# Kernel tuning notes

Hardware: AMD Instinct MI355X
Metric: run time of the kernel (lower is better)

## Reference

```python
import jax, jax.numpy as jnp
import numpy as np

BN_EPS = 1e-5


def _interpolate(xyz1, xyz2, points2):
    # squared pairwise distances [B, N, S]
    d = (jnp.sum(xyz1 ** 2, -1)[:, :, None]
         + jnp.sum(xyz2 ** 2, -1)[:, None, :]
         - 2.0 * jnp.einsum('bnc,bsc->bns', xyz1, xyz2))
    # 3 smallest distances (torch does a full sort; top-3 is the same math)
    neg_d, idx = jax.lax.top_k(-d, 3)          # [B, N, 3]
    dists = -neg_d
    w = 1.0 / (dists + 1e-8)
    w = w / jnp.sum(w, -1, keepdims=True)
    # gather points2 features at idx: [B, N, 3, D]
    gathered = jnp.take_along_axis(points2[:, None, :, :],
                                   idx[:, :, :, None], axis=2)
    return jnp.sum(gathered * w[:, :, :, None], axis=2)  # [B, N, D]


def _conv_bn_relu(x, w, b, gamma, beta):
    # x: [B, N, Cin]; 1x1 Conv1d == per-point dense layer
    y = jnp.einsum('bnc,oc->bno', x, w) + b
    mean = jnp.mean(y, axis=(0, 1))
    var = jnp.mean((y - mean) ** 2, axis=(0, 1))  # biased var (torch BN training)
    y = (y - mean) * jax.lax.rsqrt(var + BN_EPS) * gamma + beta
    return jax.nn.relu(y)


def setup_inputs() -> dict:
    key = jax.random.key(0)
    ks = jax.random.split(key, 8)
    B, N, S, D1, D2 = 8, 8192, 2048, 128, 256
    in_ch, mlp = D1 + D2, [256, 128]
    inp = {
        'xyz1': jax.random.normal(ks[0], (B, N, 3), jnp.float32),
        'xyz2': jax.random.normal(ks[1], (B, S, 3), jnp.float32),
        'points1': jax.random.normal(ks[2], (B, N, D1), jnp.float32),
        'points2': jax.random.normal(ks[3], (B, S, D2), jnp.float32),
    }
    c = in_ch
    for i, o in enumerate(mlp):
        kw = jax.random.fold_in(ks[4], i)
        inp[f'w{i}'] = jax.random.normal(kw, (o, c), jnp.float32) * (1.0 / np.sqrt(c))
        inp[f'b{i}'] = jnp.zeros((o,), jnp.float32)
        inp[f'g{i}'] = jnp.ones((o,), jnp.float32)
        inp[f'beta{i}'] = jnp.zeros((o,), jnp.float32)
        c = o
    return inp


def reference(xyz1, xyz2, points1, points2,
              w0, b0, g0, beta0, w1, b1, g1, beta1):
    interp = _interpolate(xyz1, xyz2, points2)          # [B, N, D2]
    x = jnp.concatenate([points1, interp], axis=-1)     # [B, N, D1+D2]
    x = _conv_bn_relu(x, w0, b0, g0, beta0)
    x = _conv_bn_relu(x, w1, b1, g1, beta1)
    return x                                            # [B, N, mlp[-1]]
```

## Files before the change

kernel.cpp:

```cpp
#include <hip/hip_runtime.h>
#include <hip/hip_bf16.h>

#define BATCH 8
#define NPTS  8192
#define SPTS  2048
#define D1C   128
#define D2C   256
#define C_IN  384
#define O0    256
#define O1    128
#define MROWS (BATCH * NPTS)
#define NCHUNK 8
#define CHSZ   256

typedef __attribute__((ext_vector_type(8))) short short8v;
typedef __attribute__((ext_vector_type(4))) float f32x4;

__device__ __forceinline__ unsigned short f2bf(float f) {
    union { float f; unsigned u; } v; v.f = f;
    unsigned u = v.u;
    return (unsigned short)((u + 0x7fffu + ((u >> 16) & 1u)) >> 16);
}
__device__ __forceinline__ float bf2f(unsigned short h) {
    union { unsigned u; float f; } v; v.u = ((unsigned)h) << 16;
    return v.f;
}
__device__ __forceinline__ void gload_lds16(const void* g, void* l) {
    __builtin_amdgcn_global_load_lds(
        (const __attribute__((address_space(1))) void*)g,
        (__attribute__((address_space(3))) void*)l, 16, 0, 0);
}

__global__ __launch_bounds__(256, 8) void nn3_scan(
    const float* __restrict__ xyz1, const float* __restrict__ xyz2,
    float* __restrict__ candD, int* __restrict__ candI)
{
    __shared__ float4 P[CHSZ];
    const int t  = threadIdx.x;
    const int qb = blockIdx.x;
    const int c  = blockIdx.y;
    const int b  = qb >> 5;

    {
        const float* src = xyz2 + ((size_t)b * SPTS + c * CHSZ) * 3;
        float px = src[t * 3 + 0];
        float py = src[t * 3 + 1];
        float pz = src[t * 3 + 2];
        P[t] = make_float4(px, py, pz, px * px + py * py + pz * pz);
    }
    __syncthreads();

    const int q = qb * 256 + t;
    const float* qp = xyz1 + (size_t)q * 3;
    const float qx = qp[0], qy = qp[1], qz = qp[2];
    const float qn = qx * qx + qy * qy + qz * qz;

    float d0 = 1e30f, d1 = 1e30f, d2 = 1e30f;
    int   i0 = 0,     i1 = 0,     i2 = 0;
    const int gbase = c * CHSZ;

    #pragma unroll 4
    for (int s = 0; s < CHSZ; ++s) {
        float4 p = P[s];
        float dot = qx * p.x + qy * p.y + qz * p.z;
        float d = (qn + p.w) - 2.0f * dot;
        bool c0 = d < d0, c1 = d < d1, c2 = d < d2;
        int gi = gbase + s;
        float t2 = __builtin_amdgcn_fmed3f(d, d1, d2);
        float t1 = __builtin_amdgcn_fmed3f(d, d0, d1);
        i2 = c1 ? i1 : (c2 ? gi : i2);
        i1 = c0 ? i0 : (c1 ? gi : i1);
        i0 = c0 ? gi : i0;
        d2 = t2; d1 = t1; d0 = fminf(d, d0);
    }

    const size_t base = (size_t)c * (MROWS * 3) + (size_t)q * 3;
    candD[base + 0] = d0; candD[base + 1] = d1; candD[base + 2] = d2;
    candI[base + 0] = i0; candI[base + 1] = i1; candI[base + 2] = i2;
}

__global__ __launch_bounds__(256) void nn3_merge(
    const float* __restrict__ candD, const int* __restrict__ candI,
    int* __restrict__ idx3, float* __restrict__ wgt3)
{
    const int q = blockIdx.x * 256 + threadIdx.x;

    float d0 = 1e30f, d1 = 1e30f, d2 = 1e30f;
    int   i0 = 0,     i1 = 0,     i2 = 0;

    #pragma unroll
    for (int c = 0; c < NCHUNK; ++c) {
        const size_t base = (size_t)c * (MROWS * 3) + (size_t)q * 3;
        #pragma unroll
        for (int j = 0; j < 3; ++j) {
            float d = candD[base + j];
            int  gi = candI[base + j];
            bool c0 = d < d0, c1 = d < d1, c2 = d < d2;
            float t2 = __builtin_amdgcn_fmed3f(d, d1, d2);
            float t1 = __builtin_amdgcn_fmed3f(d, d0, d1);
            i2 = c1 ? i1 : (c2 ? gi : i2);
            i1 = c0 ? i0 : (c1 ? gi : i1);
            i0 = c0 ? gi : i0;
            d2 = t2; d1 = t1; d0 = fminf(d, d0);
        }
    }

    float wa = 1.0f / (d0 + 1e-8f);
    float wb = 1.0f / (d1 + 1e-8f);
    float wc = 1.0f / (d2 + 1e-8f);
    float inv = 1.0f / (wa + wb + wc);
    wa *= inv; wb *= inv; wc *= inv;

    idx3[q * 3 + 0] = i0;
    idx3[q * 3 + 1] = i1;
    idx3[q * 3 + 2] = i2;
    wgt3[q * 3 + 0] = wa;
    wgt3[q * 3 + 1] = wb;
    wgt3[q * 3 + 2] = wc;
}

__global__ __launch_bounds__(256) void cvt_f32_bf16(
    const float* __restrict__ src, unsigned short* __restrict__ dst)
{
    int i = blockIdx.x * 256 + threadIdx.x;
    float4 v = ((const float4*)src)[i];
    ushort4 o;
    o.x = f2bf(v.x); o.y = f2bf(v.y); o.z = f2bf(v.z); o.w = f2bf(v.w);
    ((ushort4*)dst)[i] = o;
}

__global__ __launch_bounds__(256) void interp_kernel(
    const float* __restrict__ points2,
    const int* __restrict__ idx3, const float* __restrict__ wgt3,
    unsigned short* __restrict__ xI)
{
    const int w    = threadIdx.x >> 6;
    const int lane = threadIdx.x & 63;
    const int blk   = blockIdx.x;
    const int xcd   = blk & 7;
    const int local = blk >> 3;
    const int m     = (xcd * 2048 + local) * 4 + w;
    const int b     = xcd;

    const float* p2b = points2 + (size_t)b * SPTS * D2C;
    const int  gi0 = idx3[m * 3 + 0];
    const int  gi1 = idx3[m * 3 + 1];
    const int  gi2 = idx3[m * 3 + 2];
    const float w0 = wgt3[m * 3 + 0];
    const float w1 = wgt3[m * 3 + 1];
    const float w2 = wgt3[m * 3 + 2];

    float4 a  = *(const float4*)(p2b + (size_t)gi0 * D2C + lane * 4);
    float4 bb = *(const float4*)(p2b + (size_t)gi1 * D2C + lane * 4);
    float4 c  = *(const float4*)(p2b + (size_t)gi2 * D2C + lane * 4);

    ushort4 o;
    o.x = f2bf(w0 * a.x + w1 * bb.x + w2 * c.x);
    o.y = f2bf(w0 * a.y + w1 * bb.y + w2 * c.y);
    o.z = f2bf(w0 * a.z + w1 * bb.z + w2 * c.z);
    o.w = f2bf(w0 * a.w + w1 * bb.w + w2 * c.w);
    *(ushort4*)(xI + (size_t)m * D2C + lane * 4) = o;
}

__global__ __launch_bounds__(512) void gemm0_mfma(
    const float* __restrict__ points1, const unsigned short* __restrict__ xI,
    const unsigned short* __restrict__ w0bf, const float* __restrict__ b0,
    unsigned short* __restrict__ y0bf,
    float* __restrict__ sum0, float* __restrict__ sq0)
{
    __shared__ __align__(16) unsigned short As[128 * 32];
    __shared__ __align__(16) unsigned short Bs[256 * 32];

    const int t    = threadIdx.x;
    const int lane = t & 63;
    const int w    = t >> 6;
    const int wm   = w >> 2;
    const int wn   = w & 3;
    const int rowBase = blockIdx.x * 128;

    const int r      = t >> 2;
    const int ks_log = (t & 3) ^ ((t >> 3) & 3);

    const float* p1row = points1 + (size_t)(rowBase + r) * D1C;
    const unsigned short* xrow = xI + (size_t)(rowBase + r) * D2C + ks_log * 8;
    unsigned short* asw = As + t * 8;
    char* ldsA = (char*)As + w * 1024;

    const unsigned short* gB0 = w0bf + (size_t)r * C_IN + ks_log * 8;
    const unsigned short* gB1 = w0bf + (size_t)(128 + r) * C_IN + ks_log * 8;
    char* ldsB0 = (char*)Bs + w * 1024;
    char* ldsB1 = (char*)Bs + 8192 + w * 1024;

    const int rp = (lane & 15) * 64 + (((lane >> 4) ^ ((lane >> 1) & 3)) * 16);
    const char* aBase = (const char*)As + (wm * 64) * 64 + rp;
    const char* bBase = (const char*)Bs + (wn * 64) * 64 + rp;

    f32x4 acc[4][4] = {};

    for (int kt = 0; kt < C_IN / 32; ++kt) {
        gload_lds16(gB0 + kt * 32, ldsB0);
        gload_lds16(gB1 + kt * 32, ldsB1);

        if (kt < 4) {
            const int k = kt * 32 + ks_log * 8;
            float4 f0 = *(const float4*)(p1row + k);
            float4 f1 = *(const float4*)(p1row + k + 4);
            short8v av;
            av[0] = (short)f2bf(f0.x); av[1] = (short)f2bf(f0.y);
            av[2] = (short)f2bf(f0.z); av[3] = (short)f2bf(f0.w);
            av[4] = (short)f2bf(f1.x); av[5] = (short)f2bf(f1.y);
            av[6] = (short)f2bf(f1.z); av[7] = (short)f2bf(f1.w);
            *(short8v*)asw = av;
        } else {
            gload_lds16(xrow + (kt - 4) * 32, ldsA);
        }

        __syncthreads();

        short8v a[4], bf[4];
        #pragma unroll
        for (int m = 0; m < 4; ++m) a[m]  = *(const short8v*)(aBase + m * 1024);
        #pragma unroll
        for (int n = 0; n < 4; ++n) bf[n] = *(const short8v*)(bBase + n * 1024);
        #pragma unroll
        for (int m = 0; m < 4; ++m)
            #pragma unroll
            for (int n = 0; n < 4; ++n)
                acc[m][n] = __builtin_amdgcn_mfma_f32_16x16x32_bf16(
                    a[m], bf[n], acc[m][n], 0, 0, 0);

        __syncthreads();
    }

    const int colw = wn * 64 + (lane & 15);
    const int rowE = rowBase + wm * 64 + ((lane >> 4) * 4);
    float bias[4];
    #pragma unroll
    for (int n = 0; n < 4; ++n) bias[n] = b0[colw + n * 16];

    float cs[4] = {0.f, 0.f, 0.f, 0.f}, cq[4] = {0.f, 0.f, 0.f, 0.f};
    #pragma unroll
    for (int m = 0; m < 4; ++m)
        #pragma unroll
        for (int n = 0; n < 4; ++n)
            #pragma unroll
            for (int j = 0; j < 4; ++j) {
                float v = acc[m][n][j] + bias[n];
                y0bf[(size_t)(rowE + m * 16 + j) * O0 + colw + n * 16] = f2bf(v);
                cs[n] += v; cq[n] += v * v;
            }

    #pragma unroll
    for (int n = 0; n < 4; ++n) {
        float s = cs[n], qv = cq[n];
        s  += __shfl_xor(s, 16);  s  += __shfl_xor(s, 32);
        qv += __shfl_xor(qv, 16); qv += __shfl_xor(qv, 32);
        if (lane < 16) {
            atomicAdd(&sum0[colw + n * 16], s);
            atomicAdd(&sq0[colw + n * 16], qv);
        }
    }
}

__global__ void stats_kernel(const float* __restrict__ sum, const float* __restrict__ sq,
                             const float* __restrict__ g, const float* __restrict__ beta,
                             float* __restrict__ scale, float* __restrict__ shift,
                             int C, float invM)
{
    int c = blockIdx.x * blockDim.x + threadIdx.x;
    if (c < C) {
        float mean = sum[c] * invM;
        float var  = sq[c] * invM - mean * mean;
        float s = g[c] * rsqrtf(var + 1e-5f);
        scale[c] = s;
        shift[c] = beta[c] - mean * s;
    }
}

__global__ __launch_bounds__(256) void gemm1_mfma(
    const unsigned short* __restrict__ x1, const unsigned short* __restrict__ w1bf,
    const float* __restrict__ scale0, const float* __restrict__ shift0,
    const float* __restrict__ b1, unsigned short* __restrict__ y1bf,
    float* __restrict__ sum1, float* __restrict__ sq1)
{
    __shared__ __align__(16) unsigned short As[128 * 32];
    __shared__ __align__(16) unsigned short Bs[128 * 32];
    __shared__ float sc[O0], sh[O0];

    const int t    = threadIdx.x;
    const int lane = t & 63;
    const int w    = t >> 6;
    const int wm   = w >> 1, wn = w & 1;
    const int rowBase = blockIdx.x * 128;

    sc[t] = scale0[t];
    sh[t] = shift0[t];
    __syncthreads();

    const int r      = t >> 2;
    const int kl     = t & 3;
    const int kp     = kl ^ ((r >> 1) & 3);
    const int ks_log = kl ^ ((r >> 1) & 3);

    const unsigned short* gA0 = x1 + (size_t)(rowBase + r) * O0 + kl * 8;
    const unsigned short* gA1 = x1 + (size_t)(rowBase + 64 + r) * O0 + kl * 8;
    unsigned short* dA0 = As + r * 32 + kp * 8;
    unsigned short* dA1 = As + (64 + r) * 32 + kp * 8;

    const unsigned short* gB0 = w1bf + (size_t)r * O0 + ks_log * 8;
    const unsigned short* gB1 = w1bf + (size_t)(64 + r) * O0 + ks_log * 8;
    char* ldsB0 = (char*)Bs + w * 1024;
    char* ldsB1 = (char*)Bs + 4096 + w * 1024;

    const int rp = (lane & 15) * 64 + (((lane >> 4) ^ ((lane >> 1) & 3)) * 16);
    const char* aBase = (const char*)As + (wm * 64) * 64 + rp;
    const char* bBase = (const char*)Bs + (wn * 64) * 64 + rp;

    f32x4 acc[4][4] = {};

    for (int kt = 0; kt < O0 / 32; ++kt) {
        gload_lds16(gB0 + kt * 32, ldsB0);
        gload_lds16(gB1 + kt * 32, ldsB1);

        const int ch = kt * 32 + kl * 8;
        float4 s0v = *(const float4*)(sc + ch);
        float4 s1v = *(const float4*)(sc + ch + 4);
        float4 h0v = *(const float4*)(sh + ch);
        float4 h1v = *(const float4*)(sh + ch + 4);
        short8v v0 = *(const short8v*)(gA0 + kt * 32);
        short8v v1 = *(const short8v*)(gA1 + kt * 32);
        short8v o0, o1;
        o0[0] = (short)f2bf(fmaxf(0.f, bf2f((unsigned short)v0[0]) * s0v.x + h0v.x));
        o0[1] = (short)f2bf(fmaxf(0.f, bf2f((unsigned short)v0[1]) * s0v.y + h0v.y));
        o0[2] = (short)f2bf(fmaxf(0.f, bf2f((unsigned short)v0[2]) * s0v.z + h0v.z));
        o0[3] = (short)f2bf(fmaxf(0.f, bf2f((unsigned short)v0[3]) * s0v.w + h0v.w));
        o0[4] = (short)f2bf(fmaxf(0.f, bf2f((unsigned short)v0[4]) * s1v.x + h1v.x));
        o0[5] = (short)f2bf(fmaxf(0.f, bf2f((unsigned short)v0[5]) * s1v.y + h1v.y));
        o0[6] = (short)f2bf(fmaxf(0.f, bf2f((unsigned short)v0[6]) * s1v.z + h1v.z));
        o0[7] = (short)f2bf(fmaxf(0.f, bf2f((unsigned short)v0[7]) * s1v.w + h1v.w));
        o1[0] = (short)f2bf(fmaxf(0.f, bf2f((unsigned short)v1[0]) * s0v.x + h0v.x));
        o1[1] = (short)f2bf(fmaxf(0.f, bf2f((unsigned short)v1[1]) * s0v.y + h0v.y));
        o1[2] = (short)f2bf(fmaxf(0.f, bf2f((unsigned short)v1[2]) * s0v.z + h0v.z));
        o1[3] = (short)f2bf(fmaxf(0.f, bf2f((unsigned short)v1[3]) * s0v.w + h0v.w));
        o1[4] = (short)f2bf(fmaxf(0.f, bf2f((unsigned short)v1[4]) * s1v.x + h1v.x));
        o1[5] = (short)f2bf(fmaxf(0.f, bf2f((unsigned short)v1[5]) * s1v.y + h1v.y));
        o1[6] = (short)f2bf(fmaxf(0.f, bf2f((unsigned short)v1[6]) * s1v.z + h1v.z));
        o1[7] = (short)f2bf(fmaxf(0.f, bf2f((unsigned short)v1[7]) * s1v.w + h1v.w));
        *(short8v*)dA0 = o0;
        *(short8v*)dA1 = o1;

        __syncthreads();

        short8v a[4], bf[4];
        #pragma unroll
        for (int m = 0; m < 4; ++m) a[m]  = *(const short8v*)(aBase + m * 1024);
        #pragma unroll
        for (int n = 0; n < 4; ++n) bf[n] = *(const short8v*)(bBase + n * 1024);
        #pragma unroll
        for (int m = 0; m < 4; ++m)
            #pragma unroll
            for (int n = 0; n < 4; ++n)
                acc[m][n] = __builtin_amdgcn_mfma_f32_16x16x32_bf16(
                    a[m], bf[n], acc[m][n], 0, 0, 0);

        __syncthreads();
    }

    const int colw = wn * 64 + (lane & 15);
    const int rowE = rowBase + wm * 64 + ((lane >> 4) * 4);
    float bias[4];
    #pragma unroll
    for (int n = 0; n < 4; ++n) bias[n] = b1[colw + n * 16];

    float cs[4] = {0.f, 0.f, 0.f, 0.f}, cq[4] = {0.f, 0.f, 0.f, 0.f};
    #pragma unroll
    for (int m = 0; m < 4; ++m)
        #pragma unroll
        for (int n = 0; n < 4; ++n)
            #pragma unroll
            for (int j = 0; j < 4; ++j) {
                float v = acc[m][n][j] + bias[n];
                y1bf[(size_t)(rowE + m * 16 + j) * O1 + colw + n * 16] = f2bf(v);
                cs[n] += v; cq[n] += v * v;
            }

    #pragma unroll
    for (int n = 0; n < 4; ++n) {
        float s = cs[n], qv = cq[n];
        s  += __shfl_xor(s, 16);  s  += __shfl_xor(s, 32);
        qv += __shfl_xor(qv, 16); qv += __shfl_xor(qv, 32);
        if (lane < 16) {
            atomicAdd(&sum1[colw + n * 16], s);
            atomicAdd(&sq1[colw + n * 16], qv);
        }
    }
}

__global__ __launch_bounds__(256) void bn_relu_out(
    const unsigned short* __restrict__ y1bf, float* __restrict__ out,
    const float* __restrict__ scale, const float* __restrict__ shift)
{
    int i = blockIdx.x * 256 + threadIdx.x;
    short8v v = ((const short8v*)y1bf)[i];
    int c = (i * 8) & (O1 - 1);
    float4 sa = *(const float4*)(scale + c);
    float4 sb = *(const float4*)(scale + c + 4);
    float4 ha = *(const float4*)(shift + c);
    float4 hb = *(const float4*)(shift + c + 4);
    float4 o0, o1;
    o0.x = fmaxf(0.f, bf2f((unsigned short)v[0]) * sa.x + ha.x);
    o0.y = fmaxf(0.f, bf2f((unsigned short)v[1]) * sa.y + ha.y);
    o0.z = fmaxf(0.f, bf2f((unsigned short)v[2]) * sa.z + ha.z);
    o0.w = fmaxf(0.f, bf2f((unsigned short)v[3]) * sa.w + ha.w);
    o1.x = fmaxf(0.f, bf2f((unsigned short)v[4]) * sb.x + hb.x);
    o1.y = fmaxf(0.f, bf2f((unsigned short)v[5]) * sb.y + hb.y);
    o1.z = fmaxf(0.f, bf2f((unsigned short)v[6]) * sb.z + hb.z);
    o1.w = fmaxf(0.f, bf2f((unsigned short)v[7]) * sb.w + hb.w);
    ((float4*)out)[i * 2 + 0] = o0;
    ((float4*)out)[i * 2 + 1] = o1;
}

extern "C" void kernel_launch(void* const* d_in, const int* in_sizes, int n_in,
                              void* d_out, int out_size, void* d_ws, size_t ws_size,
                              hipStream_t stream)
{
    const float* xyz1    = (const float*)d_in[0];
    const float* xyz2    = (const float*)d_in[1];
    const float* points1 = (const float*)d_in[2];
    const float* points2 = (const float*)d_in[3];
    const float* w0      = (const float*)d_in[4];
    const float* b0      = (const float*)d_in[5];
    const float* g0      = (const float*)d_in[6];
    const float* beta0   = (const float*)d_in[7];
    const float* w1      = (const float*)d_in[8];
    const float* b1      = (const float*)d_in[9];
    const float* g1      = (const float*)d_in[10];
    const float* beta1   = (const float*)d_in[11];

    float* wsf = (float*)d_ws;
    float* sum0   = wsf;
    float* sq0    = wsf + 256;
    float* sum1   = wsf + 512;
    float* sq1    = wsf + 640;
    float* scale0 = wsf + 768;
    float* shift0 = wsf + 1024;
    float* scale1 = wsf + 1280;
    float* shift1 = wsf + 1408;
    unsigned short* w0bf = (unsigned short*)(wsf + 1536);
    unsigned short* w1bf = (unsigned short*)(wsf + 50688);
    float*  candD = wsf + 132608;
    int*    candI = (int*)(wsf + 1705472);
    int*    idx3  = (int*)(wsf + 3278336);
    float*  wgt3  = wsf + 3474944;
    unsigned short* y0bf = (unsigned short*)(wsf + 67072);
    unsigned short* xI   = (unsigned short*)(wsf + 8455680);
    unsigned short* y1bf = (unsigned short*)(wsf + 8455680);

    hipMemsetAsync(d_ws, 0, 768 * sizeof(float), stream);

    cvt_f32_bf16<<<(O0 * C_IN / 4) / 256, 256, 0, stream>>>(w0, w0bf);
    cvt_f32_bf16<<<(O1 * O0 / 4) / 256, 256, 0, stream>>>(w1, w1bf);

    nn3_scan<<<dim3(MROWS / 256, NCHUNK), 256, 0, stream>>>(xyz1, xyz2, candD, candI);
    nn3_merge<<<MROWS / 256, 256, 0, stream>>>(candD, candI, idx3, wgt3);

    interp_kernel<<<MROWS / 4, 256, 0, stream>>>(points2, idx3, wgt3, xI);

    gemm0_mfma<<<MROWS / 128, 512, 0, stream>>>(
        points1, xI, w0bf, b0, y0bf, sum0, sq0);

    stats_kernel<<<1, 256, 0, stream>>>(sum0, sq0, g0, beta0, scale0, shift0,
                                        O0, 1.0f / MROWS);

    gemm1_mfma<<<MROWS / 128, 256, 0, stream>>>(
        y0bf, w1bf, scale0, shift0, b1, y1bf, sum1, sq1);

    stats_kernel<<<1, 128, 0, stream>>>(sum1, sq1, g1, beta1, scale1, shift1,
                                        O1, 1.0f / MROWS);

    bn_relu_out<<<(MROWS * O1 / 8) / 256, 256, 0, stream>>>(
        y1bf, (float*)d_out, scale1, shift1);
}
```

Before: 189.4 us.

## Split kNN into distance-only pass plus threshold-pruned index pass

The top-3 search becomes two passes. The first scans all candidates tracking only distances, and a merge yields each query's global third-smallest distance. A second scan then does index bookkeeping only when some lane in the wavefront sees a distance at or below that threshold. This aims to drop the per-candidate index select work, but it adds a second full distance scan, an extra merge launch and a wave-level branch. Ties and floating-point equality could in principle pick different indices than before.

Result: slower. 201.9 us (+6.6%).

```diff
diff --git a/kernel.cpp b/kernel.cpp
--- a/kernel.cpp
+++ b/kernel.cpp
@@ -31,9 +31,9 @@
         (__attribute__((address_space(3))) void*)l, 16, 0, 0);
 }
 
-__global__ __launch_bounds__(256, 8) void nn3_scan(
+__global__ __launch_bounds__(256, 8) void nn3_scan_d(
     const float* __restrict__ xyz1, const float* __restrict__ xyz2,
-    float* __restrict__ candD, int* __restrict__ candI)
+    float* __restrict__ candD)
 {
     __shared__ float4 P[CHSZ];
     const int t  = threadIdx.x;
@@ -56,22 +56,87 @@
     const float qn = qx * qx + qy * qy + qz * qz;
 
     float d0 = 1e30f, d1 = 1e30f, d2 = 1e30f;
-    int   i0 = 0,     i1 = 0,     i2 = 0;
-    const int gbase = c * CHSZ;
-
-    #pragma unroll 4
+
+    #pragma unroll 8
     for (int s = 0; s < CHSZ; ++s) {
         float4 p = P[s];
         float dot = qx * p.x + qy * p.y + qz * p.z;
         float d = (qn + p.w) - 2.0f * dot;
-        bool c0 = d < d0, c1 = d < d1, c2 = d < d2;
-        int gi = gbase + s;
         float t2 = __builtin_amdgcn_fmed3f(d, d1, d2);
         float t1 = __builtin_amdgcn_fmed3f(d, d0, d1);
-        i2 = c1 ? i1 : (c2 ? gi : i2);
-        i1 = c0 ? i0 : (c1 ? gi : i1);
-        i0 = c0 ? gi : i0;
-        d2 = t2; d1 = t1; d0 = fminf(d, d0);
+        d0 = fminf(d, d0);
+        d1 = t1; d2 = t2;
+    }
+
+    const size_t base = (size_t)c * (MROWS * 3) + (size_t)q * 3;
+    candD[base + 0] = d0; candD[base + 1] = d1; candD[base + 2] = d2;
+}
+
+__global__ __launch_bounds__(256) void nn3_merge_d(
+    const float* __restrict__ candD, float* __restrict__ dthr)
+{
+    const int q = blockIdx.x * 256 + threadIdx.x;
+    float d0 = 1e30f, d1 = 1e30f, d2 = 1e30f;
+    #pragma unroll
+    for (int c = 0; c < NCHUNK; ++c) {
+        const size_t base = (size_t)c * (MROWS * 3) + (size_t)q * 3;
+        #pragma unroll
+        for (int j = 0; j < 3; ++j) {
+            float d = candD[base + j];
+            float t2 = __builtin_amdgcn_fmed3f(d, d1, d2);
+            float t1 = __builtin_amdgcn_fmed3f(d, d0, d1);
+            d0 = fminf(d, d0);
+            d1 = t1; d2 = t2;
+        }
+    }
+    dthr[q] = d2;
+}
+
+__global__ __launch_bounds__(256, 8) void nn3_scan_idx(
+    const float* __restrict__ xyz1, const float* __restrict__ xyz2,
+    const float* __restrict__ dthr,
+    float* __restrict__ candD, int* __restrict__ candI)
+{
+    __shared__ float4 P[CHSZ];
+    const int t  = threadIdx.x;
+    const int qb = blockIdx.x;
+    const int c  = blockIdx.y;
+    const int b  = qb >> 5;
+
+    {
+        const float* src = xyz2 + ((size_t)b * SPTS + c * CHSZ) * 3;
+        float px = src[t * 3 + 0];
+        float py = src[t * 3 + 1];
+        float pz = src[t * 3 + 2];
+        P[t] = make_float4(px, py, pz, px * px + py * py + pz * pz);
+    }
+    __syncthreads();
+
+    const int q = qb * 256 + t;
+    const float* qp = xyz1 + (size_t)q * 3;
+    const float qx = qp[0], qy = qp[1], qz = qp[2];
+    const float qn = qx * qx + qy * qy + qz * qz;
+    const float thr = dthr[q];
+
+    float d0 = 1e30f, d1 = 1e30f, d2 = 1e30f;
+    int   i0 = 0,     i1 = 0,     i2 = 0;
+    const int gbase = c * CHSZ;
+
+    #pragma unroll 2
+    for (int s = 0; s < CHSZ; ++s) {
+        float4 p = P[s];
+        float dot = qx * p.x + qy * p.y + qz * p.z;
+        float d = (qn + p.w) - 2.0f * dot;
+        if (__any(d <= thr)) {
+            bool c0 = d < d0, c1 = d < d1, c2 = d < d2;
+            int gi = gbase + s;
+            float t2 = __builtin_amdgcn_fmed3f(d, d1, d2);
+            float t1 = __builtin_amdgcn_fmed3f(d, d0, d1);
+            i2 = c1 ? i1 : (c2 ? gi : i2);
+            i1 = c0 ? i0 : (c1 ? gi : i1);
+            i0 = c0 ? gi : i0;
+            d2 = t2; d1 = t1; d0 = fminf(d, d0);
+        }
     }
 
     const size_t base = (size_t)c * (MROWS * 3) + (size_t)q * 3;
@@ -452,6 +517,7 @@
     int*    candI = (int*)(wsf + 1705472);
     int*    idx3  = (int*)(wsf + 3278336);
     float*  wgt3  = wsf + 3474944;
+    float*  dthr  = wsf + 3671552;
     unsigned short* y0bf = (unsigned short*)(wsf + 67072);
     unsigned short* xI   = (unsigned short*)(wsf + 8455680);
     unsigned short* y1bf = (unsigned short*)(wsf + 8455680);
@@ -461,7 +527,10 @@
     cvt_f32_bf16<<<(O0 * C_IN / 4) / 256, 256, 0, stream>>>(w0, w0bf);
     cvt_f32_bf16<<<(O1 * O0 / 4) / 256, 256, 0, stream>>>(w1, w1bf);
 
-    nn3_scan<<<dim3(MROWS / 256, NCHUNK), 256, 0, stream>>>(xyz1, xyz2, candD, candI);
+    nn3_scan_d<<<dim3(MROWS / 256, NCHUNK), 256, 0, stream>>>(xyz1, xyz2, candD);
+    nn3_merge_d<<<MROWS / 256, 256, 0, stream>>>(candD, dthr);
+    nn3_scan_idx<<<dim3(MROWS / 256, NCHUNK), 256, 0, stream>>>(
+        xyz1, xyz2, dthr, candD, candI);
     nn3_merge<<<MROWS / 256, 256, 0, stream>>>(candD, candI, idx3, wgt3);
 
     interp_kernel<<<MROWS / 4, 256, 0, stream>>>(points2, idx3, wgt3, xI);
```

## Double-buffer LDS tiles in both GEMM kernels to overlap loads with MFMA

Applied to the files above, without the earlier changes.

Both GEMM kernels now keep two LDS buffers for the A and B tiles. The next k-tile is issued into the alternate buffer before computing on the current one, which leaves one barrier per iteration instead of two. This is meant to hide global-to-LDS latency behind the MFMA work. It doubles LDS use, adds occupancy hints to launch_bounds, and fully unrolls the k loop, which could raise register pressure or lower occupancy.

Measured after the change: 188.6 us. About the same (-0.4%).

```diff
diff --git a/kernel.cpp b/kernel.cpp
--- a/kernel.cpp
+++ b/kernel.cpp
@@ -162,14 +162,14 @@
     *(ushort4*)(xI + (size_t)m * D2C + lane * 4) = o;
 }
 
-__global__ __launch_bounds__(512) void gemm0_mfma(
+__global__ __launch_bounds__(512, 4) void gemm0_mfma(
     const float* __restrict__ points1, const unsigned short* __restrict__ xI,
     const unsigned short* __restrict__ w0bf, const float* __restrict__ b0,
     unsigned short* __restrict__ y0bf,
     float* __restrict__ sum0, float* __restrict__ sq0)
 {
-    __shared__ __align__(16) unsigned short As[128 * 32];
-    __shared__ __align__(16) unsigned short Bs[256 * 32];
+    __shared__ __align__(16) unsigned short As[2][128 * 32];
+    __shared__ __align__(16) unsigned short Bs[2][256 * 32];
 
     const int t    = threadIdx.x;
     const int lane = t & 63;
@@ -183,24 +183,16 @@
 
     const float* p1row = points1 + (size_t)(rowBase + r) * D1C;
     const unsigned short* xrow = xI + (size_t)(rowBase + r) * D2C + ks_log * 8;
-    unsigned short* asw = As + t * 8;
-    char* ldsA = (char*)As + w * 1024;
-
     const unsigned short* gB0 = w0bf + (size_t)r * C_IN + ks_log * 8;
     const unsigned short* gB1 = w0bf + (size_t)(128 + r) * C_IN + ks_log * 8;
-    char* ldsB0 = (char*)Bs + w * 1024;
-    char* ldsB1 = (char*)Bs + 8192 + w * 1024;
 
     const int rp = (lane & 15) * 64 + (((lane >> 4) ^ ((lane >> 1) & 3)) * 16);
-    const char* aBase = (const char*)As + (wm * 64) * 64 + rp;
-    const char* bBase = (const char*)Bs + (wn * 64) * 64 + rp;
 
     f32x4 acc[4][4] = {};
 
-    for (int kt = 0; kt < C_IN / 32; ++kt) {
-        gload_lds16(gB0 + kt * 32, ldsB0);
-        gload_lds16(gB1 + kt * 32, ldsB1);
-
+    auto stage = [&](int buf, int kt) {
+        gload_lds16(gB0 + kt * 32, (char*)Bs[buf] + w * 1024);
+        gload_lds16(gB1 + kt * 32, (char*)Bs[buf] + 8192 + w * 1024);
         if (kt < 4) {
             const int k = kt * 32 + ks_log * 8;
             float4 f0 = *(const float4*)(p1row + k);
@@ -210,25 +202,34 @@
             av[2] = (short)f2bf(f0.z); av[3] = (short)f2bf(f0.w);
             av[4] = (short)f2bf(f1.x); av[5] = (short)f2bf(f1.y);
             av[6] = (short)f2bf(f1.z); av[7] = (short)f2bf(f1.w);
-            *(short8v*)asw = av;
+            *(short8v*)(As[buf] + t * 8) = av;
         } else {
-            gload_lds16(xrow + (kt - 4) * 32, ldsA);
+            gload_lds16(xrow + (kt - 4) * 32, (char*)As[buf] + w * 1024);
         }
-
-        __syncthreads();
-
-        short8v a[4], bf[4];
-        #pragma unroll
-        for (int m = 0; m < 4; ++m) a[m]  = *(const short8v*)(aBase + m * 1024);
-        #pragma unroll
-        for (int n = 0; n < 4; ++n) bf[n] = *(const short8v*)(bBase + n * 1024);
+    };
+
+    auto compute = [&](int buf) {
+        const char* aB = (const char*)As[buf] + (wm * 64) * 64 + rp;
+        const char* bB = (const char*)Bs[buf] + (wn * 64) * 64 + rp;
+        short8v a[4], bv[4];
+        #pragma unroll
+        for (int m = 0; m < 4; ++m) a[m]  = *(const short8v*)(aB + m * 1024);
+        #pragma unroll
+        for (int n = 0; n < 4; ++n) bv[n] = *(const short8v*)(bB + n * 1024);
         #pragma unroll
         for (int m = 0; m < 4; ++m)
             #pragma unroll
             for (int n = 0; n < 4; ++n)
                 acc[m][n] = __builtin_amdgcn_mfma_f32_16x16x32_bf16(
-                    a[m], bf[n], acc[m][n], 0, 0, 0);
-
+                    a[m], bv[n], acc[m][n], 0, 0, 0);
+    };
+
+    stage(0, 0);
+    __syncthreads();
+    #pragma unroll
+    for (int kt = 0; kt < C_IN / 32; ++kt) {
+        if (kt + 1 < C_IN / 32) stage((kt + 1) & 1, kt + 1);
+        compute(kt & 1);
         __syncthreads();
     }
 
@@ -277,14 +278,14 @@
     }
 }
 
-__global__ __launch_bounds__(256) void gemm1_mfma(
+__global__ __launch_bounds__(256, 2) void gemm1_mfma(
     const unsigned short* __restrict__ x1, const unsigned short* __restrict__ w1bf,
     const float* __restrict__ scale0, const float* __restrict__ shift0,
     const float* __restrict__ b1, unsigned short* __restrict__ y1bf,
     float* __restrict__ sum1, float* __restrict__ sq1)
 {
-    __shared__ __align__(16) unsigned short As[128 * 32];
-    __shared__ __align__(16) unsigned short Bs[128 * 32];
+    __shared__ __align__(16) unsigned short As[2][128 * 32];
+    __shared__ __align__(16) unsigned short Bs[2][128 * 32];
     __shared__ float sc[O0], sh[O0];
 
     const int t    = threadIdx.x;
@@ -304,23 +305,16 @@
 
     const unsigned short* gA0 = x1 + (size_t)(rowBase + r) * O0 + kl * 8;
     const unsigned short* gA1 = x1 + (size_t)(rowBase + 64 + r) * O0 + kl * 8;
-    unsigned short* dA0 = As + r * 32 + kp * 8;
-    unsigned short* dA1 = As + (64 + r) * 32 + kp * 8;
-
     const unsigned short* gB0 = w1bf + (size_t)r * O0 + ks_log * 8;
     const unsigned short* gB1 = w1bf + (size_t)(64 + r) * O0 + ks_log * 8;
-    char* ldsB0 = (char*)Bs + w * 1024;
-    char* ldsB1 = (char*)Bs + 4096 + w * 1024;
 
     const int rp = (lane & 15) * 64 + (((lane >> 4) ^ ((lane >> 1) & 3)) * 16);
-    const char* aBase = (const char*)As + (wm * 64) * 64 + rp;
-    const char* bBase = (const char*)Bs + (wn * 64) * 64 + rp;
 
     f32x4 acc[4][4] = {};
 
-    for (int kt = 0; kt < O0 / 32; ++kt) {
-        gload_lds16(gB0 + kt * 32, ldsB0);
-        gload_lds16(gB1 + kt * 32, ldsB1);
+    auto stage = [&](int buf, int kt) {
+        gload_lds16(gB0 + kt * 32, (char*)Bs[buf] + w * 1024);
+        gload_lds16(gB1 + kt * 32, (char*)Bs[buf] + 4096 + w * 1024);
 
         const int ch = kt * 32 + kl * 8;
         float4 s0v = *(const float4*)(sc + ch);
@@ -346,23 +340,32 @@
         o1[5] = (short)f2bf(fmaxf(0.f, bf2f((unsigned short)v1[5]) * s1v.y + h1v.y));
         o1[6] = (short)f2bf(fmaxf(0.f, bf2f((unsigned short)v1[6]) * s1v.z + h1v.z));
         o1[7] = (short)f2bf(fmaxf(0.f, bf2f((unsigned short)v1[7]) * s1v.w + h1v.w));
-        *(short8v*)dA0 = o0;
-        *(short8v*)dA1 = o1;
-
-        __syncthreads();
-
-        short8v a[4], bf[4];
-        #pragma unroll
-        for (int m = 0; m < 4; ++m) a[m]  = *(const short8v*)(aBase + m * 1024);
-        #pragma unroll
-        for (int n = 0; n < 4; ++n) bf[n] = *(const short8v*)(bBase + n * 1024);
+        *(short8v*)(As[buf] + r * 32 + kp * 8) = o0;
+        *(short8v*)(As[buf] + (64 + r) * 32 + kp * 8) = o1;
+    };
+
+    auto compute = [&](int buf) {
+        const char* aB = (const char*)As[buf] + (wm * 64) * 64 + rp;
+        const char* bB = (const char*)Bs[buf] + (wn * 64) * 64 + rp;
+        short8v a[4], bv[4];
+        #pragma unroll
+        for (int m = 0; m < 4; ++m) a[m]  = *(const short8v*)(aB + m * 1024);
+        #pragma unroll
+        for (int n = 0; n < 4; ++n) bv[n] = *(const short8v*)(bB + n * 1024);
         #pragma unroll
         for (int m = 0; m < 4; ++m)
             #pragma unroll
             for (int n = 0; n < 4; ++n)
                 acc[m][n] = __builtin_amdgcn_mfma_f32_16x16x32_bf16(
-                    a[m], bf[n], acc[m][n], 0, 0, 0);
-
+                    a[m], bv[n], acc[m][n], 0, 0, 0);
+    };
+
+    stage(0, 0);
+    __syncthreads();
+    #pragma unroll
+    for (int kt = 0; kt < O0 / 32; ++kt) {
+        if (kt + 1 < O0 / 32) stage((kt + 1) & 1, kt + 1);
+        compute(kt & 1);
         __syncthreads();
     }
 
```
